# Performance work log

Hardware: AMD Instinct MI355X
Metric: run time of the kernel (lower is better)

## Reference

```python
import jax, jax.numpy as jnp
import numpy as np

B, L1, L2, D = 16, 512, 512, 512
H, INNER = 8, 1024
HD = INNER // H  # 128

def _glorot(key, shape):
    fan_in, fan_out = shape[-2], shape[-1]
    lim = jnp.sqrt(6.0 / (fan_in + fan_out))
    return jax.random.uniform(key, shape, jnp.float32, -lim, lim)

def setup_inputs() -> dict:
    key = jax.random.key(0)
    ks = jax.random.split(key, 8)
    return {
        "primary": jax.random.normal(ks[0], (B, L1, D), jnp.float32),
        "secondary": jax.random.normal(ks[1], (B, L2, D), jnp.float32),
        "primary_mask": jnp.ones((B, L1), jnp.float32),
        "secondary_mask": jnp.ones((B, L2), jnp.float32),
        "W_aff": _glorot(ks[2], (H, D, D)),          # per-head bilinear affinity weights
        "W_p": _glorot(ks[3], (D, INNER)),            # linear_primary (no bias)
        "W_s": _glorot(ks[4], (D, INNER)),            # linear_secondary (no bias)
        "W_fp": _glorot(ks[5], (D + HD, D)),          # ffn_primary
        "b_fp": jnp.zeros((D,), jnp.float32),
        "W_fs": _glorot(ks[6], (D + HD, D)),          # ffn_secondary
        "b_fs": jnp.zeros((D,), jnp.float32),
    }

def reference(primary, secondary, primary_mask, secondary_mask,
              W_aff, W_p, W_s, W_fp, b_fp, W_fs, b_fs):
    b, l1, d = primary.shape
    l2 = secondary.shape[1]
    h = W_aff.shape[0]
    hd = W_p.shape[1] // h
    # affinity mask: (B, 1, L1, L2)
    mask = (primary_mask[:, :, None] * secondary_mask[:, None, :])[:, None, :, :]
    # multi-head bilinear affinity: tanh(P Wk S^T) -> (B, H, L1, L2)
    aff = jnp.tanh(jnp.einsum('bie,hef,bjf->bhij', primary, W_aff, secondary)) * mask
    # project + split heads -> (B, H, L, hd)
    pp = (primary @ W_p).reshape(b, l1, h, hd).transpose(0, 2, 1, 3)
    ps = (secondary @ W_s).reshape(b, l2, h, hd).transpose(0, 2, 1, 3)
    # weighted sums (ReLU activation)
    wp = jax.nn.relu(jnp.einsum('bhij,bhid->bhjd', aff, pp))  # (B, H, L2, hd)
    ws = jax.nn.relu(jnp.einsum('bhij,bhjd->bhid', aff, ps))  # (B, H, L1, hd)
    # GlobalMaxPool1D applied to (L, H, hd) per sample => max over heads
    pool_p = wp.max(axis=1)  # (B, L2, hd)
    pool_s = ws.max(axis=1)  # (B, L1, hd)
    out_p = jax.nn.relu(jnp.concatenate([primary, pool_s], -1) @ W_fp + b_fp)
    out_s = jax.nn.relu(jnp.concatenate([secondary, pool_p], -1) @ W_fs + b_fs)
    return out_p, out_s
```

## Files before the change

### kernel.cpp

```cpp
#include <hip/hip_runtime.h>
#include <hip/hip_bf16.h>

typedef short short8 __attribute__((ext_vector_type(8)));
typedef float f32x16 __attribute__((ext_vector_type(16)));
typedef float f32x4 __attribute__((ext_vector_type(4)));

#define BM 128
#define BN 128

typedef const __attribute__((address_space(1))) void gas_t;
typedef __attribute__((address_space(3))) void las_t;

__device__ __forceinline__ unsigned short f2bf(float f) {
  unsigned int u = __float_as_uint(f);
  u += 0x7FFFu + ((u >> 16) & 1u);
  return (unsigned short)(u >> 16);
}

__device__ __forceinline__ unsigned int pmaxu16(unsigned int a, unsigned int b) {
  unsigned int lo = ((a & 0xFFFFu) > (b & 0xFFFFu)) ? (a & 0xFFFFu) : (b & 0xFFFFu);
  unsigned int hi = ((a >> 16) > (b >> 16)) ? (a & 0xFFFF0000u) : (b & 0xFFFF0000u);
  return lo | hi;
}

__device__ __forceinline__ float fast_tanh(float x) {
  x = fminf(fmaxf(x, -10.f), 10.f);
  float t = __builtin_amdgcn_exp2f(x * 2.8853900817779268f);
  return 1.f - 2.f * __builtin_amdgcn_rcpf(t + 1.f);
}

struct GemmP {
  const unsigned short* A;
  const unsigned short* Bm;
  void* C;
  const float* A2f;
  const unsigned short* A_b;
  const unsigned short* Bm_b;
  void* C_b;
  const float* A2f_b;
  const float* mask_p;
  const float* mask_s;
  const float* bias;
  const float* bias_b;
  long long sAb, sAh, sBb, sBh, sCb, sCh;
  int lda, lda2, ldb, ldc, M, N, K, Hh, kSplit, zSplit, nbx, nby;
};

template <int TA, int EPI>
__device__ __forceinline__ void gemm_body(const GemmP& p, int bx, int by, int bz, char* smem_) {
  constexpr int PA = (TA == 0) ? 32 : 40;
  constexpr int HSA = (TA == 0) ? 4096 : 5120;
  unsigned short* As = (unsigned short*)smem_;
  unsigned short* Bs = (unsigned short*)(smem_ + 2 * HSA * 2);

  int z = bz;
  const unsigned short* Abase = p.A;
  const unsigned short* Bbase = p.Bm;
  void* Cvp = p.C;
  const float* A2f = p.A2f;
  const float* bias = p.bias;
  if (p.zSplit && z >= p.zSplit) {
    z -= p.zSplit;
    Abase = p.A_b; Bbase = p.Bm_b; Cvp = p.C_b; A2f = p.A2f_b; bias = p.bias_b;
  }
  const int zb = z / p.Hh, zh = z % p.Hh;
  const unsigned short* A = Abase + (size_t)zb * p.sAb + (size_t)zh * p.sAh;
  const unsigned short* B = Bbase + (size_t)zb * p.sBb + (size_t)zh * p.sBh;
  const int m0 = bx * BM, n0 = by * BN;
  const int tid = threadIdx.x;
  const int wid = tid >> 6, lane = tid & 63;
  const int wm = (wid >> 1) * 64, wn = (wid & 1) * 64;
  const int lrow = lane & 31;
  const int lk8 = (lane >> 5) * 8;

  f32x16 acc[2][2] = {};

  const int dm = tid >> 2, dkg = tid & 3;

  auto mfma_block = [&]() {
#pragma unroll
    for (int h = 0; h < 2; ++h)
#pragma unroll
      for (int kc = 0; kc < 2; ++kc) {
        short8 af[2], bfv[2];
#pragma unroll
        for (int mt = 0; mt < 2; ++mt)
          af[mt] = *(const short8*)&As[h * HSA + (wm + mt * 32 + lrow) * PA + kc * 16 + lk8];
#pragma unroll
        for (int nt = 0; nt < 2; ++nt)
          bfv[nt] = *(const short8*)&Bs[h * 4096 + (wn + nt * 32 + lrow) * 32 + kc * 16 + lk8];
#pragma unroll
        for (int mt = 0; mt < 2; ++mt)
#pragma unroll
          for (int nt = 0; nt < 2; ++nt)
            acc[mt][nt] = __builtin_amdgcn_mfma_f32_32x32x16_bf16(af[mt], bfv[nt], acc[mt][nt], 0, 0, 0);
      }
  };
  auto stage_b = [&](int k0) {
#pragma unroll
    for (int h = 0; h < 2; ++h)
#pragma unroll
      for (int q = 0; q < 2; ++q) {
        const unsigned short* src = B + (size_t)(n0 + q * 64 + dm) * p.ldb + (k0 + h * 32 + dkg * 8);
        __builtin_amdgcn_global_load_lds((gas_t*)src,
                                         (las_t*)&Bs[h * 4096 + q * 2048 + wid * 512],
                                         16, 0, 0);
      }
  };

  const int nIter = p.K >> 6;
  const int nIter1 = p.kSplit ? (p.kSplit >> 6) : nIter;

  for (int it = 0; it < nIter1; ++it) {
    const int k0 = it << 6;
    if (TA == 0) {
#pragma unroll
      for (int h = 0; h < 2; ++h)
#pragma unroll
        for (int q = 0; q < 2; ++q) {
          const unsigned short* src = A + (size_t)(m0 + q * 64 + dm) * p.lda + (k0 + h * 32 + dkg * 8);
          __builtin_amdgcn_global_load_lds((gas_t*)src,
                                           (las_t*)&As[h * HSA + q * 2048 + wid * 512],
                                           16, 0, 0);
        }
    } else {
      const int kk = tid & 31, mg = (tid >> 5) << 4;
#pragma unroll
      for (int h = 0; h < 2; ++h) {
        const unsigned short* src = A + (size_t)(k0 + h * 32 + kk) * p.lda + (m0 + mg);
        uint4 v0 = *(const uint4*)src;
        uint4 v1 = *(const uint4*)(src + 8);
        unsigned short tmp[16];
        *(uint4*)&tmp[0] = v0;
        *(uint4*)&tmp[8] = v1;
#pragma unroll
        for (int j = 0; j < 16; ++j) As[h * HSA + (mg + j) * PA + kk] = tmp[j];
      }
    }
    stage_b(k0);
    __syncthreads();
    mfma_block();
    __syncthreads();
  }

  if (TA == 0 && p.kSplit) {
    const unsigned short* planes = (const unsigned short*)A2f;
    for (int it = nIter1; it < nIter; ++it) {
      const int k0 = it << 6;
#pragma unroll
      for (int h2 = 0; h2 < 2; ++h2) {
        const int ko = k0 + h2 * 32 - p.kSplit;
#pragma unroll
        for (int q = 0; q < 2; ++q) {
          const int row = m0 + q * 64 + dm;
          const unsigned int* s0 = (const unsigned int*)(planes
              + ((size_t)(((row >> 9) << 12) + (row & 511)) * 128 + ko + dkg * 8));
          uint4 mv = *(const uint4*)s0;
#pragma unroll
          for (int hh = 1; hh < 8; ++hh) {
            uint4 v = *(const uint4*)(s0 + (size_t)hh * 32768);
            mv.x = pmaxu16(mv.x, v.x);
            mv.y = pmaxu16(mv.y, v.y);
            mv.z = pmaxu16(mv.z, v.z);
            mv.w = pmaxu16(mv.w, v.w);
          }
          *(uint4*)&As[h2 * HSA + (q * 64 + dm) * 32 + dkg * 8] = mv;
        }
      }
      stage_b(k0);
      __syncthreads();
      mfma_block();
      __syncthreads();
    }
  }

  unsigned short* Cu = (unsigned short*)Cvp + (size_t)zb * p.sCb + (size_t)zh * p.sCh;
  float* Cf = (float*)Cvp + (size_t)zb * p.sCb + (size_t)zh * p.sCh;

  const int rbase = 4 * (lane >> 5);

  float mp[2][16], ms[2];
  if constexpr (EPI == 1) {
#pragma unroll
    for (int mt = 0; mt < 2; ++mt)
#pragma unroll
      for (int reg = 0; reg < 16; ++reg) {
        const int rl = (reg & 3) + 8 * (reg >> 2) + rbase;
        mp[mt][reg] = p.mask_p[(size_t)zb * p.M + (m0 + wm + mt * 32 + rl)];
      }
#pragma unroll
    for (int nt = 0; nt < 2; ++nt)
      ms[nt] = p.mask_s[(size_t)zb * p.N + (n0 + wn + nt * 32 + lrow)];
  }
  if constexpr (EPI == 3) {
#pragma unroll
    for (int nt = 0; nt < 2; ++nt)
      ms[nt] = bias[n0 + wn + nt * 32 + lrow];
  }

#pragma unroll
  for (int mt = 0; mt < 2; ++mt) {
#pragma unroll
    for (int nt = 0; nt < 2; ++nt) {
      f32x16 a = acc[mt][nt];
#pragma unroll
      for (int reg = 0; reg < 16; ++reg) {
        const int rl = (reg & 3) + 8 * (reg >> 2) + rbase;
        const int grow = m0 + wm + mt * 32 + rl;
        const int gcol = n0 + wn + nt * 32 + lrow;
        const size_t idx = (size_t)grow * p.ldc + gcol;
        const float v = a[reg];
        if constexpr (EPI == 0) {
          Cu[idx] = f2bf(v);
        } else if constexpr (EPI == 1) {
          Cu[idx] = f2bf(fast_tanh(v) * (mp[mt][reg] * ms[nt]));
        } else if constexpr (EPI == 3) {
          Cf[idx] = fmaxf(v + ms[nt], 0.f);
        } else {
          Cu[idx] = f2bf(fmaxf(v, 0.f));
        }
      }
    }
  }
}

template <int TA, int EPI>
__global__ __launch_bounds__(256) void gemm_k(GemmP p) {
  extern __shared__ char smem[];
  gemm_body<TA, EPI>(p, blockIdx.x, blockIdx.y, blockIdx.z, smem);
}

template <int EPI>
__device__ __forceinline__ void gemm15_body(const GemmP& p, int bx, int by, int bz, char* smem_) {
  int z = bz;
  const unsigned short* Abase = p.A;
  const unsigned short* Bbase = p.Bm;
  void* Cvp = p.C;
  if (p.zSplit && z >= p.zSplit) {
    z -= p.zSplit;
    Abase = p.A_b; Bbase = p.Bm_b; Cvp = p.C_b;
  }
  const int zb = z / p.Hh, zh = z % p.Hh;
  const unsigned short* A = Abase + (size_t)zb * p.sAb + (size_t)zh * p.sAh;
  const unsigned short* B = Bbase + (size_t)zb * p.sBb + (size_t)zh * p.sBh;
  const int m0 = bx * 256, n0 = by * 128;
  const int tid = threadIdx.x;
  const int wid = tid >> 6, lane = tid & 63;
  const int wm = wid >> 1, wn = wid & 1;
  const int lrow = lane & 15, lhi = lane >> 4;

  const int rr = tid >> 3;
  const int cs = ((tid & 7) * 8) ^ ((rr & 7) << 3);

  const int colx = (lhi * 16) ^ ((lrow & 7) << 4);
  const int offA = (wm * 64 + lrow) * 128 + colx;
  const int offB = 32768 + (wn * 64 + lrow) * 128 + colx;

  f32x4 acc[4][4] = {};

  const int nt = p.K >> 6;

  for (int t = 0; t < nt; ++t) {
    const int k0 = t << 6;
    const unsigned short* sa = A + (size_t)(m0 + rr) * p.lda + k0 + cs;
#pragma unroll
    for (int s = 0; s < 4; ++s)
      __builtin_amdgcn_global_load_lds((gas_t*)(sa + (size_t)(s * 64) * p.lda),
                                       (las_t*)(smem_ + s * 8192 + tid * 16), 16, 0, 0);
    const unsigned short* sb = B + (size_t)(n0 + rr) * p.ldb + k0 + cs;
#pragma unroll
    for (int s = 0; s < 2; ++s)
      __builtin_amdgcn_global_load_lds((gas_t*)(sb + (size_t)(s * 64) * p.ldb),
                                       (las_t*)(smem_ + 32768 + s * 8192 + tid * 16), 16, 0, 0);
    __syncthreads();

    short8 af[4], bv[4];
#pragma unroll
    for (int fn = 0; fn < 4; ++fn) bv[fn] = *(const short8*)(smem_ + offB + fn * 2048);
#pragma unroll
    for (int fm = 0; fm < 4; ++fm) af[fm] = *(const short8*)(smem_ + offA + fm * 2048);
    __builtin_amdgcn_s_setprio(1);
#pragma unroll
    for (int fm = 0; fm < 4; ++fm)
#pragma unroll
      for (int fn = 0; fn < 4; ++fn)
        acc[fm][fn] = __builtin_amdgcn_mfma_f32_16x16x32_bf16(af[fm], bv[fn], acc[fm][fn], 0, 0, 0);
    __builtin_amdgcn_s_setprio(0);

#pragma unroll
    for (int fn = 0; fn < 4; ++fn) bv[fn] = *(const short8*)(smem_ + (offB ^ 64) + fn * 2048);
#pragma unroll
    for (int fm = 0; fm < 4; ++fm) af[fm] = *(const short8*)(smem_ + (offA ^ 64) + fm * 2048);
    __builtin_amdgcn_s_setprio(1);
#pragma unroll
    for (int fm = 0; fm < 4; ++fm)
#pragma unroll
      for (int fn = 0; fn < 4; ++fn)
        acc[fm][fn] = __builtin_amdgcn_mfma_f32_16x16x32_bf16(af[fm], bv[fn], acc[fm][fn], 0, 0, 0);
    __builtin_amdgcn_s_setprio(0);

    if (t + 1 < nt) __syncthreads();
  }

  unsigned short* Cu = (unsigned short*)Cvp + (size_t)zb * p.sCb + (size_t)zh * p.sCh;

  float ms[4];
  if constexpr (EPI == 1) {
#pragma unroll
    for (int fn = 0; fn < 4; ++fn)
      ms[fn] = p.mask_s[(size_t)zb * p.N + (n0 + wn * 64 + fn * 16 + lrow)];
  }

#pragma unroll
  for (int fm = 0; fm < 4; ++fm)
#pragma unroll
    for (int fn = 0; fn < 4; ++fn) {
      f32x4 a = acc[fm][fn];
      const int gcol = n0 + wn * 64 + fn * 16 + lrow;
#pragma unroll
      for (int reg = 0; reg < 4; ++reg) {
        const int grow = m0 + wm * 64 + fm * 16 + lhi * 4 + reg;
        const size_t idx = (size_t)grow * p.ldc + gcol;
        if constexpr (EPI == 0) {
          Cu[idx] = f2bf(a[reg]);
        } else if constexpr (EPI == 4) {
          Cu[idx] = f2bf(fmaxf(a[reg], 0.f));
        } else {
          const float mp = p.mask_p[(size_t)zb * p.M + grow];
          Cu[idx] = f2bf(fast_tanh(a[reg]) * (mp * ms[fn]));
        }
      }
    }
}

template <int EPI>
__global__ __launch_bounds__(512, 3) void gemm15_k(GemmP p) {
  extern __shared__ char smem[];
  gemm15_body<EPI>(p, blockIdx.x, blockIdx.y, blockIdx.z, smem);
}

template <int E1, int E2>
__global__ __launch_bounds__(512, 3) void gemm15_pair_k(GemmP a, GemmP b, int nA) {
  extern __shared__ char smem[];
  int bid = blockIdx.x;
  if (bid < nA) {
    const int per = a.nbx * a.nby;
    const int z = bid / per, r = bid % per;
    gemm15_body<E1>(a, r % a.nbx, r / a.nbx, z, smem);
  } else {
    bid -= nA;
    const int per = b.nbx * b.nby;
    const int z = bid / per, r = bid % per;
    gemm15_body<E2>(b, r % b.nbx, r / b.nbx, z, smem);
  }
}

__device__ __forceinline__ void trans_body(const float* src, unsigned short* dst,
                                           int R, int C, int bx, int by, float (*tile)[33]) {
  const int r0 = by * 32, c0 = bx * 32;
  const int tx = threadIdx.x & 31, ty = threadIdx.x >> 5;
#pragma unroll
  for (int j = 0; j < 4; ++j)
    tile[ty + j * 8][tx] = src[(size_t)(r0 + ty + j * 8) * C + (c0 + tx)];
  __syncthreads();
#pragma unroll
  for (int j = 0; j < 4; ++j)
    dst[(size_t)(c0 + ty + j * 8) * R + (r0 + tx)] = f2bf(tile[tx][ty + j * 8]);
}

__global__ __launch_bounds__(256) void prep_k(const float* P, const float* S,
                                              unsigned short* Pbf, unsigned short* Sbf,
                                              const float* W_aff, unsigned short* WaT,
                                              const float* W_p, unsigned short* WpT,
                                              const float* W_s, unsigned short* WsT,
                                              const float* W_fp, unsigned short* WfpT,
                                              const float* W_fs, unsigned short* WfsT) {
  __shared__ float tile[32][33];
  const int bid = blockIdx.x;
  if (bid < 8192) {
    const int n4 = 1048576;
    int i = bid * 256 + threadIdx.x;
    const float4* s = (const float4*)P;
    ushort4* d = (ushort4*)Pbf;
    if (i >= n4) { i -= n4; s = (const float4*)S; d = (ushort4*)Sbf; }
    float4 v = s[i];
    ushort4 o;
    o.x = f2bf(v.x); o.y = f2bf(v.y); o.z = f2bf(v.z); o.w = f2bf(v.w);
    d[i] = o;
  } else if (bid < 10240) {
    const int l = bid - 8192;
    const int z = l >> 8, r = l & 255;
    trans_body(W_aff + (size_t)z * 262144, WaT + (size_t)z * 262144, 512, 512,
               r & 15, r >> 4, tile);
  } else if (bid < 11264) {
    const int l = bid - 10240;
    const int z = l >> 9, r = l & 511;
    trans_body(z ? W_s : W_p, z ? WsT : WpT, 512, 1024, r & 31, r >> 5, tile);
  } else {
    const int l = bid - 11264;
    const int z = l / 320, r = l % 320;
    trans_body(z ? W_fs : W_fp, z ? WfsT : WfpT, 640, 512, r & 15, r >> 4, tile);
  }
}

extern "C" void kernel_launch(void* const* d_in, const int* in_sizes, int n_in,
                              void* d_out, int out_size, void* d_ws, size_t ws_size,
                              hipStream_t stream) {
  (void)in_sizes; (void)n_in; (void)out_size; (void)ws_size;
  const float* primary   = (const float*)d_in[0];
  const float* secondary = (const float*)d_in[1];
  const float* pmask     = (const float*)d_in[2];
  const float* smask     = (const float*)d_in[3];
  const float* W_aff     = (const float*)d_in[4];
  const float* W_p       = (const float*)d_in[5];
  const float* W_s       = (const float*)d_in[6];
  const float* W_fp      = (const float*)d_in[7];
  const float* b_fp      = (const float*)d_in[8];
  const float* W_fs      = (const float*)d_in[9];
  const float* b_fs      = (const float*)d_in[10];

  constexpr int Bb = 16, L = 512, Dd = 512, Hh = 8, HDd = 128, INNER = 1024, CAT = 640;
  constexpr int NT = Hh * Dd;
  constexpr long long LD = (long long)L * Dd;
  constexpr long long LL = (long long)L * L;

  static bool s_attr = [] {
    hipFuncSetAttribute(reinterpret_cast<const void*>(&gemm15_pair_k<0, 0>),
                        hipFuncAttributeMaxDynamicSharedMemorySize, 49152);
    hipFuncSetAttribute(reinterpret_cast<const void*>(&gemm15_k<1>),
                        hipFuncAttributeMaxDynamicSharedMemorySize, 49152);
    hipFuncSetAttribute(reinterpret_cast<const void*>(&gemm15_k<4>),
                        hipFuncAttributeMaxDynamicSharedMemorySize, 49152);
    return true;
  }();
  (void)s_attr;

  char* base = (char*)d_ws;
  size_t off = 0;
  auto alloc = [&](size_t bytes) -> void* {
    void* r = base + off;
    off += (bytes + 255) & ~(size_t)255;
    return r;
  };

  unsigned short* Pbf   = (unsigned short*)alloc((size_t)Bb * L * Dd * 2);
  unsigned short* Sbf   = (unsigned short*)alloc((size_t)Bb * L * Dd * 2);
  unsigned short* WaT   = (unsigned short*)alloc((size_t)NT * Dd * 2);
  unsigned short* WpT   = (unsigned short*)alloc((size_t)INNER * Dd * 2);
  unsigned short* WsT   = (unsigned short*)alloc((size_t)INNER * Dd * 2);
  unsigned short* WfpT  = (unsigned short*)alloc((size_t)Dd * CAT * 2);
  unsigned short* WfsT  = (unsigned short*)alloc((size_t)Dd * CAT * 2);
  unsigned short* psT   = (unsigned short*)alloc((size_t)Bb * INNER * L * 2);
  unsigned short* ppT   = (unsigned short*)alloc((size_t)Bb * INNER * L * 2);
  unsigned short* Tbuf  = (unsigned short*)alloc((size_t)Bb * L * NT * 2);
  unsigned short* affb  = (unsigned short*)alloc((size_t)Bb * Hh * L * L * 2);

  unsigned short* wsBuf = Tbuf;
  unsigned short* wpBuf = Tbuf + (size_t)Bb * Hh * L * HDd;

  prep_k<<<dim3(11904), dim3(256), 0, stream>>>(primary, secondary, Pbf, Sbf,
                                                W_aff, WaT, W_p, WpT, W_s, WsT,
                                                W_fp, WfpT, W_fs, WfsT);

  {
    GemmP a{};
    a.A = Pbf; a.lda = Dd;
    a.Bm = WaT; a.ldb = Dd;
    a.C = Tbuf; a.ldc = NT;
    a.M = Bb * L; a.N = NT; a.K = Dd; a.Hh = 1; a.nbx = 32; a.nby = 32;

    GemmP b{};
    b.A = WsT; b.lda = Dd; b.sAb = 0;
    b.Bm = Sbf; b.ldb = Dd; b.sBb = LD;
    b.C = psT; b.ldc = L; b.sCb = (long long)INNER * L;
    b.A_b = WpT; b.Bm_b = Pbf; b.C_b = ppT;
    b.M = INNER; b.N = L; b.K = Dd; b.Hh = 1; b.zSplit = Bb; b.nbx = 4; b.nby = 4;

    gemm15_pair_k<0, 0><<<dim3(1024 + 512), dim3(512), 49152, stream>>>(a, b, 1024);
  }

  {
    GemmP g{};
    g.A = Tbuf; g.lda = NT; g.sAb = (long long)L * NT; g.sAh = Dd;
    g.Bm = Sbf; g.ldb = Dd; g.sBb = LD; g.sBh = 0;
    g.C = affb; g.ldc = L; g.sCb = (long long)Hh * LL; g.sCh = LL;
    g.mask_p = pmask; g.mask_s = smask;
    g.M = L; g.N = L; g.K = Dd; g.Hh = Hh;
    gemm15_k<1><<<dim3(2, 4, Bb * Hh), dim3(512), 49152, stream>>>(g);
  }

  {
    GemmP a{};
    a.A = affb; a.lda = L; a.sAb = (long long)Hh * LL; a.sAh = LL;
    a.Bm = psT; a.ldb = L; a.sBb = (long long)INNER * L; a.sBh = (long long)HDd * L;
    a.C = wsBuf; a.ldc = HDd; a.sCb = (long long)Hh * L * HDd; a.sCh = (long long)L * HDd;
    a.M = L; a.N = HDd; a.K = L; a.Hh = Hh;
    gemm15_k<4><<<dim3(2, 1, Bb * Hh), dim3(512), 49152, stream>>>(a);
  }

  {
    GemmP b{};
    b.A = affb; b.lda = L; b.sAb = (long long)Hh * LL; b.sAh = LL;
    b.Bm = ppT; b.ldb = L; b.sBb = (long long)INNER * L; b.sBh = (long long)HDd * L;
    b.C = wpBuf; b.ldc = HDd; b.sCb = (long long)Hh * L * HDd; b.sCh = (long long)L * HDd;
    b.M = L; b.N = HDd; b.K = L; b.Hh = Hh;
    gemm_k<1, 4><<<dim3(4, 1, Bb * Hh), dim3(256), 36864, stream>>>(b);
  }

  {
    GemmP g{};
    g.A = Pbf; g.lda = Dd;
    g.A2f = (const float*)wsBuf; g.lda2 = HDd; g.kSplit = Dd;
    g.Bm = WfpT; g.ldb = CAT;
    g.C = d_out; g.ldc = Dd;
    g.bias = b_fp;
    g.A_b = Sbf; g.A2f_b = (const float*)wpBuf; g.Bm_b = WfsT;
    g.C_b = (float*)d_out + (size_t)Bb * L * Dd;
    g.bias_b = b_fs;
    g.M = Bb * L; g.N = Dd; g.K = CAT; g.Hh = 1; g.zSplit = 1;
    gemm_k<0, 3><<<dim3(64, 4, 2), dim3(256), 32768, stream>>>(g);
  }
}
```

Before: 299.4 us.

## Double-buffer A tiles in LDS and load B fragments directly from global

The 256x128 GEMM kernel now runs 4 waves of 256 threads instead of 8, each wave computing a 128x64 sub-tile with 8x4 accumulators. A tiles are double-buffered in LDS, with the next K-step prefetched while the current one computes. B fragments are read straight from global memory into registers, so B no longer needs a second barrier or LDS staging. The aim is to overlap load latency with MFMA work and remove one sync per iteration, at the cost of higher register pressure, lower occupancy and uncoalesced direct B loads.

```diff
diff --git a/kernel.cpp b/kernel.cpp
--- a/kernel.cpp
+++ b/kernel.cpp
@@ -231,7 +231,7 @@
 }
 
 template <int EPI>
-__device__ __forceinline__ void gemm15_body(const GemmP& p, int bx, int by, int bz, char* smem_) {
+__device__ __forceinline__ void gemm17_body(const GemmP& p, int bx, int by, int bz, char* smem_) {
   int z = bz;
   const unsigned short* Abase = p.A;
   const unsigned short* Bbase = p.Bm;
@@ -253,53 +253,60 @@
   const int cs = ((tid & 7) * 8) ^ ((rr & 7) << 3);
 
   const int colx = (lhi * 16) ^ ((lrow & 7) << 4);
-  const int offA = (wm * 64 + lrow) * 128 + colx;
-  const int offB = 32768 + (wn * 64 + lrow) * 128 + colx;
-
-  f32x4 acc[4][4] = {};
+  const int offA = (wm * 128 + lrow) * 128 + colx;
+
+  const unsigned short* Brow = B + (size_t)(n0 + wn * 64 + lrow) * p.ldb + lhi * 8;
+
+  f32x4 acc[8][4] = {};
+
+  auto stageA = [&](int t, int slot) {
+    const int k0 = t << 6;
+    const unsigned short* sa = A + (size_t)(m0 + rr) * p.lda + k0 + cs;
+#pragma unroll
+    for (int s = 0; s < 8; ++s)
+      __builtin_amdgcn_global_load_lds((gas_t*)(sa + (size_t)(s * 32) * p.lda),
+                                       (las_t*)(smem_ + slot * 32768 + s * 4096 + tid * 16),
+                                       16, 0, 0);
+  };
 
   const int nt = p.K >> 6;
+  stageA(0, 0);
 
   for (int t = 0; t < nt; ++t) {
     const int k0 = t << 6;
-    const unsigned short* sa = A + (size_t)(m0 + rr) * p.lda + k0 + cs;
-#pragma unroll
-    for (int s = 0; s < 4; ++s)
-      __builtin_amdgcn_global_load_lds((gas_t*)(sa + (size_t)(s * 64) * p.lda),
-                                       (las_t*)(smem_ + s * 8192 + tid * 16), 16, 0, 0);
-    const unsigned short* sb = B + (size_t)(n0 + rr) * p.ldb + k0 + cs;
-#pragma unroll
-    for (int s = 0; s < 2; ++s)
-      __builtin_amdgcn_global_load_lds((gas_t*)(sb + (size_t)(s * 64) * p.ldb),
-                                       (las_t*)(smem_ + 32768 + s * 8192 + tid * 16), 16, 0, 0);
-    __syncthreads();
-
-    short8 af[4], bv[4];
-#pragma unroll
-    for (int fn = 0; fn < 4; ++fn) bv[fn] = *(const short8*)(smem_ + offB + fn * 2048);
-#pragma unroll
-    for (int fm = 0; fm < 4; ++fm) af[fm] = *(const short8*)(smem_ + offA + fm * 2048);
-    __builtin_amdgcn_s_setprio(1);
-#pragma unroll
-    for (int fm = 0; fm < 4; ++fm)
+
+    short8 bq[2][4];
+#pragma unroll
+    for (int ks = 0; ks < 2; ++ks)
 #pragma unroll
       for (int fn = 0; fn < 4; ++fn)
-        acc[fm][fn] = __builtin_amdgcn_mfma_f32_16x16x32_bf16(af[fm], bv[fn], acc[fm][fn], 0, 0, 0);
-    __builtin_amdgcn_s_setprio(0);
-
-#pragma unroll
-    for (int fn = 0; fn < 4; ++fn) bv[fn] = *(const short8*)(smem_ + (offB ^ 64) + fn * 2048);
-#pragma unroll
-    for (int fm = 0; fm < 4; ++fm) af[fm] = *(const short8*)(smem_ + (offA ^ 64) + fm * 2048);
-    __builtin_amdgcn_s_setprio(1);
-#pragma unroll
-    for (int fm = 0; fm < 4; ++fm)
-#pragma unroll
-      for (int fn = 0; fn < 4; ++fn)
-        acc[fm][fn] = __builtin_amdgcn_mfma_f32_16x16x32_bf16(af[fm], bv[fn], acc[fm][fn], 0, 0, 0);
-    __builtin_amdgcn_s_setprio(0);
-
-    if (t + 1 < nt) __syncthreads();
+        bq[ks][fn] = *(const short8*)(Brow + (size_t)(fn * 16) * p.ldb + k0 + ks * 32);
+
+    asm volatile("s_waitcnt vmcnt(8)" ::: "memory");
+    __builtin_amdgcn_s_barrier();
+    __builtin_amdgcn_sched_barrier(0);
+
+    if (t + 1 < nt) stageA(t + 1, (t + 1) & 1);
+
+    const char* sb = smem_ + (t & 1) * 32768;
+#pragma unroll
+    for (int ks = 0; ks < 2; ++ks) {
+#pragma unroll
+      for (int mh = 0; mh < 2; ++mh) {
+        short8 af[4];
+#pragma unroll
+        for (int fm = 0; fm < 4; ++fm)
+          af[fm] = *(const short8*)(sb + (offA ^ (ks * 64)) + (mh * 4 + fm) * 2048);
+        __builtin_amdgcn_s_setprio(1);
+#pragma unroll
+        for (int fm = 0; fm < 4; ++fm)
+#pragma unroll
+          for (int fn = 0; fn < 4; ++fn)
+            acc[mh * 4 + fm][fn] =
+                __builtin_amdgcn_mfma_f32_16x16x32_bf16(af[fm], bq[ks][fn], acc[mh * 4 + fm][fn], 0, 0, 0);
+        __builtin_amdgcn_s_setprio(0);
+      }
+    }
   }
 
   unsigned short* Cu = (unsigned short*)Cvp + (size_t)zb * p.sCb + (size_t)zh * p.sCh;
@@ -312,14 +319,14 @@
   }
 
 #pragma unroll
-  for (int fm = 0; fm < 4; ++fm)
+  for (int fm = 0; fm < 8; ++fm)
 #pragma unroll
     for (int fn = 0; fn < 4; ++fn) {
       f32x4 a = acc[fm][fn];
       const int gcol = n0 + wn * 64 + fn * 16 + lrow;
 #pragma unroll
       for (int reg = 0; reg < 4; ++reg) {
-        const int grow = m0 + wm * 64 + fm * 16 + lhi * 4 + reg;
+        const int grow = m0 + wm * 128 + fm * 16 + lhi * 4 + reg;
         const size_t idx = (size_t)grow * p.ldc + gcol;
         if constexpr (EPI == 0) {
           Cu[idx] = f2bf(a[reg]);
@@ -334,24 +341,24 @@
 }
 
 template <int EPI>
-__global__ __launch_bounds__(512, 3) void gemm15_k(GemmP p) {
+__global__ __launch_bounds__(256, 2) void gemm17_k(GemmP p) {
   extern __shared__ char smem[];
-  gemm15_body<EPI>(p, blockIdx.x, blockIdx.y, blockIdx.z, smem);
+  gemm17_body<EPI>(p, blockIdx.x, blockIdx.y, blockIdx.z, smem);
 }
 
 template <int E1, int E2>
-__global__ __launch_bounds__(512, 3) void gemm15_pair_k(GemmP a, GemmP b, int nA) {
+__global__ __launch_bounds__(256, 2) void gemm17_pair_k(GemmP a, GemmP b, int nA) {
   extern __shared__ char smem[];
   int bid = blockIdx.x;
   if (bid < nA) {
     const int per = a.nbx * a.nby;
     const int z = bid / per, r = bid % per;
-    gemm15_body<E1>(a, r % a.nbx, r / a.nbx, z, smem);
+    gemm17_body<E1>(a, r % a.nbx, r / a.nbx, z, smem);
   } else {
     bid -= nA;
     const int per = b.nbx * b.nby;
     const int z = bid / per, r = bid % per;
-    gemm15_body<E2>(b, r % b.nbx, r / b.nbx, z, smem);
+    gemm17_body<E2>(b, r % b.nbx, r / b.nbx, z, smem);
   }
 }
 
@@ -425,12 +432,12 @@
   constexpr long long LL = (long long)L * L;
 
   static bool s_attr = [] {
-    hipFuncSetAttribute(reinterpret_cast<const void*>(&gemm15_pair_k<0, 0>),
-                        hipFuncAttributeMaxDynamicSharedMemorySize, 49152);
-    hipFuncSetAttribute(reinterpret_cast<const void*>(&gemm15_k<1>),
-                        hipFuncAttributeMaxDynamicSharedMemorySize, 49152);
-    hipFuncSetAttribute(reinterpret_cast<const void*>(&gemm15_k<4>),
-                        hipFuncAttributeMaxDynamicSharedMemorySize, 49152);
+    hipFuncSetAttribute(reinterpret_cast<const void*>(&gemm17_pair_k<0, 0>),
+                        hipFuncAttributeMaxDynamicSharedMemorySize, 65536);
+    hipFuncSetAttribute(reinterpret_cast<const void*>(&gemm17_k<1>),
+                        hipFuncAttributeMaxDynamicSharedMemorySize, 65536);
+    hipFuncSetAttribute(reinterpret_cast<const void*>(&gemm17_k<4>),
+                        hipFuncAttributeMaxDynamicSharedMemorySize, 65536);
     return true;
   }();
   (void)s_attr;
@@ -476,7 +483,7 @@
     b.A_b = WpT; b.Bm_b = Pbf; b.C_b = ppT;
     b.M = INNER; b.N = L; b.K = Dd; b.Hh = 1; b.zSplit = Bb; b.nbx = 4; b.nby = 4;
 
-    gemm15_pair_k<0, 0><<<dim3(1024 + 512), dim3(512), 49152, stream>>>(a, b, 1024);
+    gemm17_pair_k<0, 0><<<dim3(1024 + 512), dim3(256), 65536, stream>>>(a, b, 1024);
   }
 
   {
@@ -486,7 +493,7 @@
     g.C = affb; g.ldc = L; g.sCb = (long long)Hh * LL; g.sCh = LL;
     g.mask_p = pmask; g.mask_s = smask;
     g.M = L; g.N = L; g.K = Dd; g.Hh = Hh;
-    gemm15_k<1><<<dim3(2, 4, Bb * Hh), dim3(512), 49152, stream>>>(g);
+    gemm17_k<1><<<dim3(2, 4, Bb * Hh), dim3(256), 65536, stream>>>(g);
   }
 
   {
@@ -495,7 +502,7 @@
     a.Bm = psT; a.ldb = L; a.sBb = (long long)INNER * L; a.sBh = (long long)HDd * L;
     a.C = wsBuf; a.ldc = HDd; a.sCb = (long long)Hh * L * HDd; a.sCh = (long long)L * HDd;
     a.M = L; a.N = HDd; a.K = L; a.Hh = Hh;
-    gemm15_k<4><<<dim3(2, 1, Bb * Hh), dim3(512), 49152, stream>>>(a);
+    gemm17_k<4><<<dim3(2, 1, Bb * Hh), dim3(256), 65536, stream>>>(a);
   }
 
   {
```

Result: slower. 328.4 us (+9.7%).

## Add 256x256-tile double-buffered GEMM for projection and affinity kernels

Applied to the files above, without the earlier changes.

Introduces a new GEMM body with 256x256 output tiles, 128KB of double-buffered LDS filled by direct global-to-LDS loads, and interleaved barriers with MFMA priority raising. It replaces the 128x128 kernels for the fused projection pair and the tanh-masked affinity GEMM, halving the block count. The goal is more operand reuse per byte loaded and overlap of loads with MFMA work. In exchange, occupancy drops to two blocks per CU with heavy LDS use, and there are fewer blocks to fill the machine.

```diff
diff --git a/kernel.cpp b/kernel.cpp
--- a/kernel.cpp
+++ b/kernel.cpp
@@ -339,19 +339,174 @@
   gemm15_body<EPI>(p, blockIdx.x, blockIdx.y, blockIdx.z, smem);
 }
 
+#define VMW4() asm volatile("s_waitcnt vmcnt(4)" ::: "memory")
+#define VMW0() asm volatile("s_waitcnt vmcnt(0)" ::: "memory")
+#define SBAR() do { __builtin_amdgcn_s_barrier(); __builtin_amdgcn_sched_barrier(0); } while (0)
+
+template <int EPI>
+__device__ __forceinline__ void gemm20_body(const GemmP& p, int bx, int by, int bz, char* smem_) {
+  int z = bz;
+  const unsigned short* Abase = p.A;
+  const unsigned short* Bbase = p.Bm;
+  void* Cvp = p.C;
+  if (p.zSplit && z >= p.zSplit) {
+    z -= p.zSplit;
+    Abase = p.A_b; Bbase = p.Bm_b; Cvp = p.C_b;
+  }
+  const int zb = z / p.Hh, zh = z % p.Hh;
+  const unsigned short* A = Abase + (size_t)zb * p.sAb + (size_t)zh * p.sAh;
+  const unsigned short* B = Bbase + (size_t)zb * p.sBb + (size_t)zh * p.sBh;
+  const int m0 = bx * 256, n0 = by * 256;
+  const int tid = threadIdx.x;
+  const int wid = tid >> 6, lane = tid & 63;
+  const int wm = wid >> 2, wn = wid & 3;
+  const int lrow = lane & 15, lhi = lane >> 4;
+
+  const int rr = tid >> 3;
+  const int cs = ((tid & 7) * 8) ^ ((rr & 7) << 3);
+
+  const int colx = (lhi * 16) ^ ((lrow & 7) << 4);
+  const int offA = wm * 16384 + lrow * 128 + colx;
+  const int offB = 32768 + (wn >> 1) * 16384 + ((wn & 1) * 64 + lrow) * 128 + colx;
+
+  f32x4 acc[8][4] = {};
+
+  auto stageA = [&](int t, int h) {
+    const unsigned short* s = A + (size_t)(m0 + h * 128 + rr) * p.lda + (t << 6) + cs;
+    char* d = smem_ + (t & 1) * 65536 + h * 16384 + tid * 16;
+    __builtin_amdgcn_global_load_lds((gas_t*)s, (las_t*)d, 16, 0, 0);
+    __builtin_amdgcn_global_load_lds((gas_t*)(s + (size_t)64 * p.lda), (las_t*)(d + 8192), 16, 0, 0);
+  };
+  auto stageB = [&](int t, int h) {
+    const unsigned short* s = B + (size_t)(n0 + h * 128 + rr) * p.ldb + (t << 6) + cs;
+    char* d = smem_ + (t & 1) * 65536 + 32768 + h * 16384 + tid * 16;
+    __builtin_amdgcn_global_load_lds((gas_t*)s, (las_t*)d, 16, 0, 0);
+    __builtin_amdgcn_global_load_lds((gas_t*)(s + (size_t)64 * p.ldb), (las_t*)(d + 8192), 16, 0, 0);
+  };
+
+  const int nt = p.K >> 6;
+
+  stageA(0, 0); stageA(0, 1); stageB(0, 0); stageB(0, 1);
+  stageA(1, 0); stageA(1, 1);
+  VMW4();
+  SBAR();
+
+  for (int t = 0; t < nt; ++t) {
+    const char* sb = smem_ + (t & 1) * 65536;
+    short8 af[4], bv[4];
+
+#pragma unroll
+    for (int fn = 0; fn < 4; ++fn) bv[fn] = *(const short8*)(sb + offB + fn * 2048);
+#pragma unroll
+    for (int fm = 0; fm < 4; ++fm) af[fm] = *(const short8*)(sb + offA + fm * 2048);
+    if (t + 1 < nt) stageB(t + 1, 0);
+    SBAR();
+    __builtin_amdgcn_s_setprio(1);
+#pragma unroll
+    for (int fm = 0; fm < 4; ++fm)
+#pragma unroll
+      for (int fn = 0; fn < 4; ++fn)
+        acc[fm][fn] = __builtin_amdgcn_mfma_f32_16x16x32_bf16(af[fm], bv[fn], acc[fm][fn], 0, 0, 0);
+    __builtin_amdgcn_s_setprio(0);
+    SBAR();
+
+#pragma unroll
+    for (int fm = 0; fm < 4; ++fm) af[fm] = *(const short8*)(sb + offA + 8192 + fm * 2048);
+    if (t + 1 < nt) stageB(t + 1, 1);
+    SBAR();
+    __builtin_amdgcn_s_setprio(1);
+#pragma unroll
+    for (int fm = 0; fm < 4; ++fm)
+#pragma unroll
+      for (int fn = 0; fn < 4; ++fn)
+        acc[4 + fm][fn] = __builtin_amdgcn_mfma_f32_16x16x32_bf16(af[fm], bv[fn], acc[4 + fm][fn], 0, 0, 0);
+    __builtin_amdgcn_s_setprio(0);
+    SBAR();
+
+#pragma unroll
+    for (int fn = 0; fn < 4; ++fn) bv[fn] = *(const short8*)(sb + ((offB + fn * 2048) ^ 64));
+#pragma unroll
+    for (int fm = 0; fm < 4; ++fm) af[fm] = *(const short8*)(sb + ((offA + fm * 2048) ^ 64));
+    SBAR();
+    __builtin_amdgcn_s_setprio(1);
+#pragma unroll
+    for (int fm = 0; fm < 4; ++fm)
+#pragma unroll
+      for (int fn = 0; fn < 4; ++fn)
+        acc[fm][fn] = __builtin_amdgcn_mfma_f32_16x16x32_bf16(af[fm], bv[fn], acc[fm][fn], 0, 0, 0);
+    __builtin_amdgcn_s_setprio(0);
+    SBAR();
+
+#pragma unroll
+    for (int fm = 0; fm < 4; ++fm) af[fm] = *(const short8*)(sb + ((offA + 8192 + fm * 2048) ^ 64));
+    SBAR();
+    __builtin_amdgcn_s_setprio(1);
+#pragma unroll
+    for (int fm = 0; fm < 4; ++fm)
+#pragma unroll
+      for (int fn = 0; fn < 4; ++fn)
+        acc[4 + fm][fn] = __builtin_amdgcn_mfma_f32_16x16x32_bf16(af[fm], bv[fn], acc[4 + fm][fn], 0, 0, 0);
+    __builtin_amdgcn_s_setprio(0);
+    SBAR();
+
+    if (t + 2 < nt) { stageA(t + 2, 0); stageA(t + 2, 1); }
+    if (t + 1 < nt) {
+      if (t + 2 < nt) VMW4(); else VMW0();
+      SBAR();
+    }
+  }
+
+  unsigned short* Cu = (unsigned short*)Cvp + (size_t)zb * p.sCb + (size_t)zh * p.sCh;
+
+  float ms[4];
+  if constexpr (EPI == 1) {
+#pragma unroll
+    for (int fn = 0; fn < 4; ++fn)
+      ms[fn] = p.mask_s[(size_t)zb * p.N + (n0 + wn * 64 + fn * 16 + lrow)];
+  }
+
+#pragma unroll
+  for (int fm = 0; fm < 8; ++fm)
+#pragma unroll
+    for (int fn = 0; fn < 4; ++fn) {
+      f32x4 a = acc[fm][fn];
+      const int gcol = n0 + wn * 64 + fn * 16 + lrow;
+#pragma unroll
+      for (int reg = 0; reg < 4; ++reg) {
+        const int grow = m0 + wm * 128 + fm * 16 + lhi * 4 + reg;
+        const size_t idx = (size_t)grow * p.ldc + gcol;
+        if constexpr (EPI == 0) {
+          Cu[idx] = f2bf(a[reg]);
+        } else {
+          const float mp = p.mask_p[(size_t)zb * p.M + grow];
+          Cu[idx] = f2bf(fast_tanh(a[reg]) * (mp * ms[fn]));
+        }
+      }
+    }
+}
+
+template <int EPI>
+__global__ __launch_bounds__(512, 2) void gemm20_k(GemmP p) {
+  extern __shared__ char smem[];
+  const int bid = blockIdx.x;
+  const int per = p.nbx * p.nby;
+  const int z = bid / per, r = bid % per;
+  gemm20_body<EPI>(p, r % p.nbx, r / p.nbx, z, smem);
+}
+
 template <int E1, int E2>
-__global__ __launch_bounds__(512, 3) void gemm15_pair_k(GemmP a, GemmP b, int nA) {
+__global__ __launch_bounds__(512, 2) void gemm20_pair_k(GemmP a, GemmP b, int nA) {
   extern __shared__ char smem[];
   int bid = blockIdx.x;
   if (bid < nA) {
     const int per = a.nbx * a.nby;
     const int z = bid / per, r = bid % per;
-    gemm15_body<E1>(a, r % a.nbx, r / a.nbx, z, smem);
+    gemm20_body<E1>(a, r % a.nbx, r / a.nbx, z, smem);
   } else {
     bid -= nA;
     const int per = b.nbx * b.nby;
     const int z = bid / per, r = bid % per;
-    gemm15_body<E2>(b, r % b.nbx, r / b.nbx, z, smem);
+    gemm20_body<E2>(b, r % b.nbx, r / b.nbx, z, smem);
   }
 }
 
@@ -425,10 +580,10 @@
   constexpr long long LL = (long long)L * L;
 
   static bool s_attr = [] {
-    hipFuncSetAttribute(reinterpret_cast<const void*>(&gemm15_pair_k<0, 0>),
-                        hipFuncAttributeMaxDynamicSharedMemorySize, 49152);
-    hipFuncSetAttribute(reinterpret_cast<const void*>(&gemm15_k<1>),
-                        hipFuncAttributeMaxDynamicSharedMemorySize, 49152);
+    hipFuncSetAttribute(reinterpret_cast<const void*>(&gemm20_pair_k<0, 0>),
+                        hipFuncAttributeMaxDynamicSharedMemorySize, 131072);
+    hipFuncSetAttribute(reinterpret_cast<const void*>(&gemm20_k<1>),
+                        hipFuncAttributeMaxDynamicSharedMemorySize, 131072);
     hipFuncSetAttribute(reinterpret_cast<const void*>(&gemm15_k<4>),
                         hipFuncAttributeMaxDynamicSharedMemorySize, 49152);
     return true;
@@ -467,16 +622,16 @@
     a.A = Pbf; a.lda = Dd;
     a.Bm = WaT; a.ldb = Dd;
     a.C = Tbuf; a.ldc = NT;
-    a.M = Bb * L; a.N = NT; a.K = Dd; a.Hh = 1; a.nbx = 32; a.nby = 32;
+    a.M = Bb * L; a.N = NT; a.K = Dd; a.Hh = 1; a.nbx = 32; a.nby = 16;
 
     GemmP b{};
     b.A = WsT; b.lda = Dd; b.sAb = 0;
     b.Bm = Sbf; b.ldb = Dd; b.sBb = LD;
     b.C = psT; b.ldc = L; b.sCb = (long long)INNER * L;
     b.A_b = WpT; b.Bm_b = Pbf; b.C_b = ppT;
-    b.M = INNER; b.N = L; b.K = Dd; b.Hh = 1; b.zSplit = Bb; b.nbx = 4; b.nby = 4;
-
-    gemm15_pair_k<0, 0><<<dim3(1024 + 512), dim3(512), 49152, stream>>>(a, b, 1024);
+    b.M = INNER; b.N = L; b.K = Dd; b.Hh = 1; b.zSplit = Bb; b.nbx = 4; b.nby = 2;
+
+    gemm20_pair_k<0, 0><<<dim3(512 + 256), dim3(512), 131072, stream>>>(a, b, 512);
   }
 
   {
@@ -485,8 +640,8 @@
     g.Bm = Sbf; g.ldb = Dd; g.sBb = LD; g.sBh = 0;
     g.C = affb; g.ldc = L; g.sCb = (long long)Hh * LL; g.sCh = LL;
     g.mask_p = pmask; g.mask_s = smask;
-    g.M = L; g.N = L; g.K = Dd; g.Hh = Hh;
-    gemm15_k<1><<<dim3(2, 4, Bb * Hh), dim3(512), 49152, stream>>>(g);
+    g.M = L; g.N = L; g.K = Dd; g.Hh = Hh; g.nbx = 2; g.nby = 2;
+    gemm20_k<1><<<dim3(4 * Bb * Hh), dim3(512), 131072, stream>>>(g);
   }
 
   {
```

Result: no change. 300.2 us (+0.3%).
